# Kernel optimization log

Hardware: AMD Instinct MI355X
Metric: run time of the kernel (lower is better)

## Reference

```python
import jax, jax.numpy as jnp
import numpy as np

N = 4096
FIN = 4096
LOC = 16
H1, H2, HEADS = 120, 50, 4
H1_PER = H1 // HEADS
FILM_Z = 32
SSDB_H = 60
N_HEMI = N // 2
NEG_SLOPE = 0.1
GATE_BIAS = -2.0
MASK_FILL = -9e15


def leaky(x):
    return jax.nn.leaky_relu(x, negative_slope=NEG_SLOPE)


def gat(x, mask, W, a_src, a_dst, bias, concat):
    # x: (N, Fin), W: (H, Fin, O), a_src/a_dst: (H, O), mask: (N, N) bool
    wh = jnp.einsum('nf,hfo->hno', x, W)            # (H, N, O)
    f1 = jnp.einsum('hno,ho->hn', wh, a_src)        # (H, N)
    f2 = jnp.einsum('hno,ho->hn', wh, a_dst)        # (H, N)
    e = leaky(f1[:, :, None] + f2[:, None, :])      # (H, N, N)
    e = jnp.where(mask[None], e, MASK_FILL)
    alpha = jax.nn.softmax(e, axis=-1)
    out = jnp.einsum('hij,hjo->hio', alpha, wh)     # (H, N, O)
    if concat:
        h, n, o = out.shape
        out2 = out.transpose(1, 0, 2).reshape(n, h * o)
    else:
        out2 = out.mean(axis=0)
    return out2 + bias


def _uni(k, shape, stdv):
    return jax.random.uniform(k, shape, jnp.float32, -stdv, stdv)


def setup_inputs() -> dict:
    key = jax.random.key(0)
    ks = jax.random.split(key, 30)
    s1 = 1.0 / np.sqrt(H1_PER)
    s2 = 1.0 / np.sqrt(H2)
    inp = {
        'x_fc': jax.random.normal(ks[0], (N, FIN), jnp.float32),
        'adj': jax.random.randint(ks[1], (N, N), 0, 2, jnp.int32),
        'l_loc': jax.random.uniform(ks[2], (N, LOC), jnp.float32),
        # gat1
        'W1': _uni(ks[3], (HEADS, FIN, H1_PER), s1),
        'a1s': _uni(ks[4], (HEADS, H1_PER), s1),
        'a1d': _uni(ks[5], (HEADS, H1_PER), s1),
        'b1': _uni(ks[6], (H1,), s1),
        # gat2
        'W2': _uni(ks[7], (1, H1, H2), s2),
        'a2s': _uni(ks[8], (1, H2), s2),
        'a2d': _uni(ks[9], (1, H2), s2),
        'b2': _uni(ks[10], (H2,), s2),
        # classifier (no bias)
        'Wc': _uni(ks[11], (2, H2), s2),
        # FiLM trunk
        'Wl1': _uni(ks[12], (FILM_Z, LOC), 1.0 / np.sqrt(LOC)),
        'bl1': _uni(ks[13], (FILM_Z,), 1.0 / np.sqrt(LOC)),
        'Wl2': _uni(ks[14], (FILM_Z, FILM_Z), 1.0 / np.sqrt(FILM_Z)),
        'bl2': _uni(ks[15], (FILM_Z,), 1.0 / np.sqrt(FILM_Z)),
        'Wg': _uni(ks[16], (H2, FILM_Z), 1.0 / np.sqrt(FILM_Z)),
        'bg': _uni(ks[17], (H2,), 1.0 / np.sqrt(FILM_Z)),
        'Wb': _uni(ks[18], (H2, FILM_Z), 1.0 / np.sqrt(FILM_Z)),
        'bb': _uni(ks[19], (H2,), 1.0 / np.sqrt(FILM_Z)),
        'Wgate': _uni(ks[20], (1, FILM_Z), 1.0 / np.sqrt(FILM_Z)),
        'bgate': jnp.full((1,), GATE_BIAS, jnp.float32),
        # SSDB hemi
        'Ws1': _uni(ks[21], (SSDB_H, N_HEMI), 1.0 / np.sqrt(N_HEMI)),
        'bs1': _uni(ks[22], (SSDB_H,), 1.0 / np.sqrt(N_HEMI)),
        'Ws2': _uni(ks[23], (1, SSDB_H), 1.0 / np.sqrt(SSDB_H)),
        'bs2': _uni(ks[24], (1,), 1.0 / np.sqrt(SSDB_H)),
    }
    return inp


def reference(x_fc, adj, l_loc, W1, a1s, a1d, b1, W2, a2s, a2d, b2, Wc,
              Wl1, bl1, Wl2, bl2, Wg, bg, Wb, bb, Wgate, bgate,
              Ws1, bs1, Ws2, bs2):
    mask = adj > 0
    h = leaky(gat(x_fc, mask, W1, a1s, a1d, b1, concat=True))    # (N, 120)
    h = leaky(gat(h, mask, W2, a2s, a2d, b2, concat=False))      # (N, 50)
    # FiLM conditioning
    z = leaky(l_loc @ Wl1.T + bl1)
    z = leaky(z @ Wl2.T + bl2)
    gamma = z @ Wg.T + bg                                        # (N, 50)
    beta = z @ Wb.T + bb                                         # (N, 50)
    g = jax.nn.sigmoid(z @ Wgate.T + bgate)                      # (N, 1)
    cov = jnp.clip(l_loc[:, -1], 0.0, 1.0)                       # coverage_power = 1.0
    g = g * cov[:, None]
    h_fused = h + g * (gamma * h + beta)
    logits = leaky(h_fused @ Wc.T)                               # (N, 2)
    # hemisphere SSDB bias
    t = logits.T                                                 # (2, N)
    ipsi = t[:, :N_HEMI]
    contra = t[:, N_HEMI:2 * N_HEMI]
    h_i = leaky(ipsi @ Ws1.T + bs1)                              # (2, 60)
    h_c = leaky(contra @ Ws1.T + bs1)
    b_i = leaky(h_i @ Ws2.T + bs2)                               # (2, 1)
    b_c = leaky(h_c @ Ws2.T + bs2)
    b_mid = 0.5 * (b_i + b_c)                                    # (2, 1)
    bias_nodes = jnp.concatenate([
        jnp.broadcast_to(b_i.T, (N_HEMI, 2)),
        jnp.broadcast_to(b_c.T, (N_HEMI, 2)),
    ], axis=0)                                                   # n_mid = 0
    logits = logits + bias_nodes
    bias_avg = b_mid[:, 0]                                       # (2,)
    return logits, bias_avg
```

## Files before the change

### kernel.cpp

```cpp
#include <hip/hip_runtime.h>

#define NN 4096
#define HEADS 4
#define H1PER 30
#define H1DIM 120
#define H2DIM 50

typedef short short8_t __attribute__((ext_vector_type(8)));
typedef float f32x4 __attribute__((ext_vector_type(4)));

__device__ __forceinline__ float lrelu(float x) { return x > 0.f ? x : 0.1f * x; }

__device__ __forceinline__ unsigned short bfrne(float x) {
  unsigned u = __float_as_uint(x);
  u += 0x7fffu + ((u >> 16) & 1u);
  return (unsigned short)(u >> 16);
}
__device__ __forceinline__ unsigned bfpk_rne(float lo, float hi) {
  return (unsigned)bfrne(lo) | ((unsigned)bfrne(hi) << 16);
}
__device__ __forceinline__ unsigned bfpk(float lo, float hi) {
  unsigned a = (__float_as_uint(lo) + 0x8000u) >> 16;
  unsigned b = (__float_as_uint(hi) + 0x8000u) & 0xffff0000u;
  return a | b;
}

#define GL16(g, l)                                                                        \
  __builtin_amdgcn_global_load_lds((const __attribute__((address_space(1))) unsigned int*)(g), \
                                   (__attribute__((address_space(3))) unsigned int*)(l), 16, 0, 0)

__global__ __launch_bounds__(256) void k_bits(const int* __restrict__ adj,
                                              unsigned long long* __restrict__ bits) {
  size_t base = (size_t)blockIdx.x * 1024;
  int t = threadIdx.x;
  int v0 = adj[base + t];
  int v1 = adj[base + 256 + t];
  int v2 = adj[base + 512 + t];
  int v3 = adj[base + 768 + t];
  unsigned long long m0 = __ballot(v0 > 0);
  unsigned long long m1 = __ballot(v1 > 0);
  unsigned long long m2 = __ballot(v2 > 0);
  unsigned long long m3 = __ballot(v3 > 0);
  if ((t & 63) == 0) {
    size_t w = (base + t) >> 6;
    bits[w] = m0;
    bits[w + 4] = m1;
    bits[w + 8] = m2;
    bits[w + 12] = m3;
  }
}

__global__ __launch_bounds__(256) void k_prep(const float* __restrict__ W1,
                                              const float* __restrict__ a1s,
                                              const float* __restrict__ a1d,
                                              unsigned short* __restrict__ w1t) {
  int k = blockIdx.x * 256 + threadIdx.x;
#pragma unroll
  for (int h = 0; h < 4; ++h) {
    const float* wp = W1 + ((size_t)h * 4096 + k) * H1PER;
    float fs = 0.f, fd = 0.f;
#pragma unroll
    for (int oo = 0; oo < H1PER; ++oo) {
      float v = wp[oo];
      w1t[(size_t)(h * 30 + oo) * 4096 + k] = bfrne(v);
      fs += v * a1s[h * H1PER + oo];
      fd += v * a1d[h * H1PER + oo];
    }
    w1t[(size_t)(120 + h) * 4096 + k] = bfrne(fs);
    w1t[(size_t)(124 + h) * 4096 + k] = bfrne(fd);
  }
}

__global__ __launch_bounds__(256) void k_gemm1s(const float* __restrict__ x,
                                                const unsigned short* __restrict__ w1t,
                                                float* __restrict__ part) {
  const int t = threadIdx.x;
  const int lane = t & 63, wave = t >> 6;
  const int m = lane & 15, q = lane >> 4;
  const int i0 = blockIdx.x * 32;
  const int kz = blockIdx.y * 512;
  __shared__ float xs[32 * 64];
  const int r0 = (wave & 1) * 16;
  const int ntg0 = (wave >> 1) * 4;
  const int srow0 = wave * 8 + q;
  const int srow1 = srow0 + 4;
  const int sc0 = m ^ (srow0 & 7);
  const int sc1 = m ^ (srow1 & 7);
  const float* gx0 = x + (size_t)(i0 + srow0) * 4096 + kz + sc0 * 4;
  const float* gx1 = x + (size_t)(i0 + srow1) * 4096 + kz + sc1 * 4;
  float* ls0 = &xs[srow0 * 64 + m * 4];
  float* ls1 = &xs[srow1 * 64 + m * 4];
  const int arow = r0 + m;
  const int asw = (m & 7);
  f32x4 acc[4];
#pragma unroll
  for (int nt = 0; nt < 4; ++nt) acc[nt] = (f32x4){0.f, 0.f, 0.f, 0.f};
  for (int it = 0; it < 8; ++it) {
    const int kc = it * 64;
    GL16(gx0 + kc, ls0);
    GL16(gx1 + kc, ls1);
    __syncthreads();
#pragma unroll
    for (int ks2 = 0; ks2 < 2; ++ks2) {
      const int c0 = ks2 * 8 + q * 2;
      float4 a0 = *(const float4*)&xs[arow * 64 + ((c0 ^ asw) * 4)];
      float4 a1 = *(const float4*)&xs[arow * 64 + (((c0 + 1) ^ asw) * 4)];
      union { short8_t v; unsigned u[4]; } A;
      A.u[0] = bfpk_rne(a0.x, a0.y);
      A.u[1] = bfpk_rne(a0.z, a0.w);
      A.u[2] = bfpk_rne(a1.x, a1.y);
      A.u[3] = bfpk_rne(a1.z, a1.w);
      const unsigned short* wp = w1t + (size_t)m * 4096 + kz + kc + ks2 * 32 + q * 8;
#pragma unroll
      for (int nt = 0; nt < 4; ++nt) {
        short8_t B = *(const short8_t*)(wp + (size_t)(ntg0 + nt) * 16 * 4096);
        acc[nt] = __builtin_amdgcn_mfma_f32_16x16x32_bf16(A.v, B, acc[nt], 0, 0, 0);
      }
    }
    __syncthreads();
  }
  float* pp = part + ((size_t)blockIdx.y * 4096 + i0 + r0 + q * 4) * 128 + ntg0 * 16 + m;
#pragma unroll
  for (int nt = 0; nt < 4; ++nt)
#pragma unroll
    for (int r = 0; r < 4; ++r) pp[r * 128 + nt * 16] = acc[nt][r];
}

__global__ __launch_bounds__(256) void k_f1c(const float* __restrict__ part,
                                             unsigned short* __restrict__ whbt,
                                             float* __restrict__ f1, float* __restrict__ f2) {
  const int t = threadIdx.x;
  const int n = blockIdx.x * 16 + (t >> 4);
  const int og = (t & 15) * 8;
  float s[8] = {0.f, 0.f, 0.f, 0.f, 0.f, 0.f, 0.f, 0.f};
  for (int z = 0; z < 8; ++z) {
    const float* pp = part + ((size_t)z * NN + n) * 128 + og;
    float4 u0 = *(const float4*)pp;
    float4 u1 = *(const float4*)(pp + 4);
    s[0] += u0.x; s[1] += u0.y; s[2] += u0.z; s[3] += u0.w;
    s[4] += u1.x; s[5] += u1.y; s[6] += u1.z; s[7] += u1.w;
  }
  if (og < 120) {
#pragma unroll
    for (int j = 0; j < 8; ++j) {
      int o = og + j;
      int h = o / 30, oo = o - h * 30;
      whbt[(size_t)(h * 32 + oo) * NN + n] = bfrne(s[j]);
    }
  } else {
#pragma unroll
    for (int j = 0; j < 4; ++j) {
      f1[(size_t)j * NN + n] = s[j];
      f2[(size_t)j * NN + n] = s[4 + j];
    }
  }
  if ((t & 15) < 8) {
    int h = (t & 15) >> 1, odd = (t & 15) & 1;
    whbt[(size_t)(h * 32 + 30 + odd) * NN + n] = odd ? 0 : 0x3f80;
  }
}

__global__ __launch_bounds__(256) void k_max(const float* __restrict__ v, float* __restrict__ mx) {
  int t = threadIdx.x;
  const float* row = v + (size_t)blockIdx.x * NN;
  float m = -3.0e38f;
  for (int n = t; n < NN; n += 256) m = fmaxf(m, row[n]);
  for (int off = 32; off > 0; off >>= 1) m = fmaxf(m, __shfl_down(m, off));
  __shared__ float ms[4];
  if ((t & 63) == 0) ms[t >> 6] = m;
  __syncthreads();
  if (t == 0) mx[blockIdx.x] = fmaxf(fmaxf(ms[0], ms[1]), fmaxf(ms[2], ms[3]));
}

__global__ __launch_bounds__(256) void k_att1m(const unsigned short* __restrict__ whbt,
                                               const float* __restrict__ f1, const float* __restrict__ f2,
                                               const float* __restrict__ mx,
                                               const unsigned int* __restrict__ bits32,
                                               float* __restrict__ part) {
  const int h = blockIdx.y, js = blockIdx.z;
  const int t = threadIdx.x;
  const int lane = t & 63, wave = t >> 6;
  const int m = lane & 15, q = lane >> 4;
  const int i0 = blockIdx.x * 64 + wave * 16;
  const int jbase = js * 1024;
  const float mxh = mx[h];
  __shared__ float2 es[1024];
  for (int e = t; e < 1024; e += 256) {
    float fv = f2[h * NN + jbase + e] - mxh;
    es[e] = make_float2(__expf(fv), __expf(0.1f * fv));
  }
  __syncthreads();
  const float f1r = f1[h * NN + i0 + m];
  const float s = f1r + mxh;
  const float C1 = __expf(fminf(0.f, 0.9f * s));
  const float C2 = __expf(fminf(0.f, -0.9f * s));
  const float Tr = __expf(-s);
  const unsigned int* brow = bits32 + (size_t)(i0 + m) * 128 + (jbase >> 5);
  const unsigned short* bb0 = whbt + (size_t)(h * 32 + m) * NN + jbase + q * 8;
  const unsigned short* bb1 = bb0 + 16 * NN;
  const float2* fp = es + q * 8;
  f32x4 acc0 = {0.f, 0.f, 0.f, 0.f}, acc1 = {0.f, 0.f, 0.f, 0.f};
  for (int step = 0; step < 32; ++step) {
    const int jl = step * 32;
    unsigned bsel = brow[step] >> (q * 8);
    float4 e01 = *(const float4*)(fp + jl);
    float4 e23 = *(const float4*)(fp + jl + 2);
    float4 e45 = *(const float4*)(fp + jl + 4);
    float4 e67 = *(const float4*)(fp + jl + 6);
    auto sc = [&](float ep, float en, int jj) {
      float wv = (ep > Tr) ? C1 * ep : C2 * en;
      return ((bsel >> jj) & 1u) ? wv : 0.f;
    };
    float w0 = sc(e01.x, e01.y, 0);
    float w1 = sc(e01.z, e01.w, 1);
    float w2 = sc(e23.x, e23.y, 2);
    float w3 = sc(e23.z, e23.w, 3);
    float w4 = sc(e45.x, e45.y, 4);
    float w5 = sc(e45.z, e45.w, 5);
    float w6 = sc(e67.x, e67.y, 6);
    float w7 = sc(e67.z, e67.w, 7);
    union { short8_t v; unsigned u[4]; } A;
    A.u[0] = bfpk(w0, w1);
    A.u[1] = bfpk(w2, w3);
    A.u[2] = bfpk(w4, w5);
    A.u[3] = bfpk(w6, w7);
    short8_t b0 = *(const short8_t*)(bb0 + jl);
    short8_t b1 = *(const short8_t*)(bb1 + jl);
    acc0 = __builtin_amdgcn_mfma_f32_16x16x32_bf16(A.v, b0, acc0, 0, 0, 0);
    acc1 = __builtin_amdgcn_mfma_f32_16x16x32_bf16(A.v, b1, acc1, 0, 0, 0);
  }
  float* pp = part + ((size_t)(js * 4 + h) * NN + i0 + q * 4) * 32 + m;
#pragma unroll
  for (int r = 0; r < 4; ++r) {
    pp[r * 32] = acc0[r];
    pp[r * 32 + 16] = acc1[r];
  }
}

__global__ __launch_bounds__(256) void k_h1(const float* __restrict__ part, const float* __restrict__ b1,
                                            float* __restrict__ h1) {
  int t = threadIdx.x;
  int lane = t & 63;
  int p = lane >> 5, o = lane & 31;
  int id = blockIdx.x * 8 + (t >> 6) * 2 + p;
  int h = id >> 12, n = id & 4095;
  float tot = 0.f;
#pragma unroll
  for (int z = 0; z < 4; ++z) tot += part[((size_t)(z * 4 + h) * NN + n) * 32 + o];
  float l = __shfl(tot, p * 32 + 30);
  if (o < H1PER) h1[(size_t)n * H1DIM + h * H1PER + o] = lrelu(tot / l + b1[h * H1PER + o]);
}

__global__ __launch_bounds__(256) void k_gemm2(const float* __restrict__ h1, const float* __restrict__ W2,
                                               float* __restrict__ wh2) {
  const int n0 = blockIdx.x * 4;
  const int t = threadIdx.x;
  const int o = t & 63, r = t >> 6;
  __shared__ float hs[4][120];
  for (int e = t; e < 4 * H1DIM; e += 256) hs[e / H1DIM][e % H1DIM] = h1[(size_t)n0 * H1DIM + e];
  __syncthreads();
  if (o < H2DIM) {
    float acc = 0.f;
#pragma unroll 4
    for (int k = 0; k < H1DIM; ++k) acc += hs[r][k] * W2[k * H2DIM + o];
    wh2[(size_t)(n0 + r) * H2DIM + o] = acc;
  }
}

__global__ __launch_bounds__(256) void k_f2l2(const float* __restrict__ wh2, const float* __restrict__ a2s,
                                              const float* __restrict__ a2d, float* __restrict__ f1,
                                              float* __restrict__ f2, unsigned short* __restrict__ whbt) {
  int n = blockIdx.x * 256 + threadIdx.x;
  if (n >= NN) return;
  const float* r = wh2 + (size_t)n * H2DIM;
  unsigned short* wb = whbt + n;
  float accs = 0.f, accd = 0.f;
#pragma unroll
  for (int j = 0; j < H2DIM; ++j) {
    float v = r[j];
    wb[j * NN] = bfrne(v);
    accs += v * a2s[j];
    accd += v * a2d[j];
  }
  wb[50 * NN] = 0x3f80;
#pragma unroll
  for (int j = 51; j < 64; ++j) wb[j * NN] = 0;
  f1[n] = accs;
  f2[n] = accd;
}

__global__ __launch_bounds__(256) void k_att2m(const unsigned short* __restrict__ whbt,
                                               const float* __restrict__ f1, const float* __restrict__ f2,
                                               const float* __restrict__ mx,
                                               const unsigned int* __restrict__ bits32,
                                               float* __restrict__ part) {
  const int js = blockIdx.y;
  const int t = threadIdx.x;
  const int lane = t & 63, wave = t >> 6;
  const int m = lane & 15, q = lane >> 4;
  const int i0 = blockIdx.x * 64 + wave * 16;
  const int jbase = js * 512;
  const float mx0 = mx[0];
  __shared__ float2 es[512];
  for (int e = t; e < 512; e += 256) {
    float fv = f2[jbase + e] - mx0;
    es[e] = make_float2(__expf(fv), __expf(0.1f * fv));
  }
  __syncthreads();
  const float f1r = f1[i0 + m];
  const float s = f1r + mx0;
  const float C1 = __expf(fminf(0.f, 0.9f * s));
  const float C2 = __expf(fminf(0.f, -0.9f * s));
  const float Tr = __expf(-s);
  const unsigned int* brow = bits32 + (size_t)(i0 + m) * 128 + (jbase >> 5);
  const unsigned short* bb = whbt + (size_t)m * NN + jbase + q * 8;
  const float2* fp = es + q * 8;
  f32x4 acc[4];
#pragma unroll
  for (int x = 0; x < 4; ++x) acc[x] = (f32x4){0.f, 0.f, 0.f, 0.f};
  for (int step = 0; step < 16; ++step) {
    const int jl = step * 32;
    unsigned bsel = brow[step] >> (q * 8);
    float4 e01 = *(const float4*)(fp + jl);
    float4 e23 = *(const float4*)(fp + jl + 2);
    float4 e45 = *(const float4*)(fp + jl + 4);
    float4 e67 = *(const float4*)(fp + jl + 6);
    auto sc = [&](float ep, float en, int jj) {
      float wv = (ep > Tr) ? C1 * ep : C2 * en;
      return ((bsel >> jj) & 1u) ? wv : 0.f;
    };
    float w0 = sc(e01.x, e01.y, 0);
    float w1 = sc(e01.z, e01.w, 1);
    float w2 = sc(e23.x, e23.y, 2);
    float w3 = sc(e23.z, e23.w, 3);
    float w4 = sc(e45.x, e45.y, 4);
    float w5 = sc(e45.z, e45.w, 5);
    float w6 = sc(e67.x, e67.y, 6);
    float w7 = sc(e67.z, e67.w, 7);
    union { short8_t v; unsigned u[4]; } A;
    A.u[0] = bfpk(w0, w1);
    A.u[1] = bfpk(w2, w3);
    A.u[2] = bfpk(w4, w5);
    A.u[3] = bfpk(w6, w7);
#pragma unroll
    for (int tile = 0; tile < 4; ++tile) {
      short8_t b = *(const short8_t*)(bb + (size_t)tile * 16 * NN + jl);
      acc[tile] = __builtin_amdgcn_mfma_f32_16x16x32_bf16(A.v, b, acc[tile], 0, 0, 0);
    }
  }
  float* pp = part + ((size_t)js * NN + i0 + q * 4) * 64 + m;
#pragma unroll
  for (int tile = 0; tile < 4; ++tile)
#pragma unroll
    for (int r = 0; r < 4; ++r) pp[r * 64 + tile * 16] = acc[tile][r];
}

__global__ __launch_bounds__(256) void k_h2(const float* __restrict__ part, const float* __restrict__ b2,
                                            float* __restrict__ h2) {
  int t = threadIdx.x;
  int n = blockIdx.x * 4 + (t >> 6);
  int o = t & 63;
  const float* p = part + (size_t)n * 64 + o;
  float tot = 0.f;
#pragma unroll
  for (int z = 0; z < 8; ++z) tot += p[(size_t)z * NN * 64];
  float l = __shfl(tot, 50);
  if (o < H2DIM) h2[(size_t)n * H2DIM + o] = lrelu(tot / l + b2[o]);
}

__global__ __launch_bounds__(256) void k_film(const float* __restrict__ l_loc, const float* __restrict__ h2,
                                              const float* __restrict__ Wl1, const float* __restrict__ bl1,
                                              const float* __restrict__ Wl2, const float* __restrict__ bl2,
                                              const float* __restrict__ Wg, const float* __restrict__ bg,
                                              const float* __restrict__ Wb, const float* __restrict__ bb,
                                              const float* __restrict__ Wgate, const float* __restrict__ bgate,
                                              const float* __restrict__ Wc, float* __restrict__ logits) {
  int n = blockIdx.x * 4 + (threadIdx.x >> 6);
  int lane = threadIdx.x & 63;
  int r32 = lane & 31;
  float locv = l_loc[n * 16 + (lane & 15)];
  float cov = __shfl(locv, 15);
  cov = fminf(fmaxf(cov, 0.f), 1.f);
  float a1v = bl1[r32];
#pragma unroll
  for (int j = 0; j < 16; ++j) a1v += Wl1[r32 * 16 + j] * __shfl(locv, j);
  float z1 = lrelu(a1v);
  float a2v = bl2[r32];
#pragma unroll
  for (int j = 0; j < 32; ++j) a2v += Wl2[r32 * 32 + j] * __shfl(z1, j);
  float z2 = lrelu(a2v);
  float gs = bgate[0];
  float gam, bet;
  {
    int o = lane < H2DIM ? lane : 0;
    gam = bg[o];
    bet = bb[o];
#pragma unroll
    for (int j = 0; j < 32; ++j) {
      float zj = __shfl(z2, j);
      gs += Wgate[j] * zj;
      gam += Wg[o * 32 + j] * zj;
      bet += Wb[o * 32 + j] * zj;
    }
  }
  float g = cov / (1.f + __expf(-gs));
  int o = lane < H2DIM ? lane : 0;
  float hv = h2[(size_t)n * H2DIM + o];
  float hf = hv + g * (gam * hv + bet);
  float p0 = lane < H2DIM ? hf * Wc[o] : 0.f;
  float p1 = lane < H2DIM ? hf * Wc[H2DIM + o] : 0.f;
  for (int off = 32; off > 0; off >>= 1) {
    p0 += __shfl_down(p0, off);
    p1 += __shfl_down(p1, off);
  }
  if (lane == 0) {
    logits[n * 2 + 0] = lrelu(p0);
    logits[n * 2 + 1] = lrelu(p1);
  }
}

__global__ __launch_bounds__(64) void k_ssdb1(const float* __restrict__ logits, const float* __restrict__ Ws1,
                                              float* __restrict__ hsum) {
  int combo = blockIdx.y;
  int hemi = combo >> 1, c = combo & 1;
  int k = threadIdx.x;
  if (k >= 60) return;
  int nbase = blockIdx.x * 256;
  const float* wrow = Ws1 + (size_t)k * 2048 + nbase;
  const float* lcol = logits + (size_t)(hemi * 2048 + nbase) * 2 + c;
  float part = 0.f;
  for (int q = 0; q < 256; ++q) part += wrow[q] * lcol[2 * q];
  atomicAdd(&hsum[combo * 60 + k], part);
}

__global__ __launch_bounds__(256) void k_ssdb2(const float* __restrict__ hsum, const float* __restrict__ bs1,
                                               const float* __restrict__ Ws2, const float* __restrict__ bs2,
                                               float* __restrict__ B) {
  int t = threadIdx.x;
  int combo = t >> 6, k = t & 63;
  float part = 0.f;
  if (k < 60) part = lrelu(hsum[combo * 60 + k] + bs1[k]) * Ws2[k];
  for (int off = 32; off > 0; off >>= 1) part += __shfl_down(part, off);
  if (k == 0) B[combo] = lrelu(part + bs2[0]);
}

__global__ __launch_bounds__(256) void k_final(const float* __restrict__ logits, const float* __restrict__ B,
                                               float* __restrict__ out) {
  int id = blockIdx.x * 256 + threadIdx.x;
  if (id < 2 * NN) {
    int n = id >> 1, c = id & 1;
    out[id] = logits[id] + B[(n < 2048 ? 0 : 2) + c];
  } else if (id < 2 * NN + 2) {
    int c = id - 2 * NN;
    out[id] = 0.5f * (B[c] + B[2 + c]);
  }
}

#define OFF_BITS 0
#define OFF_W1T 524288
#define OFF_GP 786432
#define OFF_A1P 786432
#define OFF_A2P 786432
#define OFF_H1 2883584
#define OFF_WH2 3375104
#define OFF_WH2BT 3579904
#define OFF_F12 3710976
#define OFF_F22 3715072
#define OFF_MX2 3719168
#define OFF_H2 3719232
#define OFF_LOG 3924032
#define OFF_HSUM 3932224
#define OFF_B 3932480
#define OFF_WH1BT 9175040
#define OFF_F1A 9437184
#define OFF_F2A 9453568
#define OFF_MX1 9469952

extern "C" void kernel_launch(void* const* d_in, const int* in_sizes, int n_in,
                              void* d_out, int out_size, void* d_ws, size_t ws_size,
                              hipStream_t stream) {
  const float* x_fc  = (const float*)d_in[0];
  const int*   adj   = (const int*)d_in[1];
  const float* l_loc = (const float*)d_in[2];
  const float* W1    = (const float*)d_in[3];
  const float* a1s   = (const float*)d_in[4];
  const float* a1d   = (const float*)d_in[5];
  const float* b1    = (const float*)d_in[6];
  const float* W2    = (const float*)d_in[7];
  const float* a2s   = (const float*)d_in[8];
  const float* a2d   = (const float*)d_in[9];
  const float* b2    = (const float*)d_in[10];
  const float* Wc    = (const float*)d_in[11];
  const float* Wl1   = (const float*)d_in[12];
  const float* bl1   = (const float*)d_in[13];
  const float* Wl2   = (const float*)d_in[14];
  const float* bl2   = (const float*)d_in[15];
  const float* Wg    = (const float*)d_in[16];
  const float* bg    = (const float*)d_in[17];
  const float* Wb    = (const float*)d_in[18];
  const float* bb    = (const float*)d_in[19];
  const float* Wgate = (const float*)d_in[20];
  const float* bgate = (const float*)d_in[21];
  const float* Ws1   = (const float*)d_in[22];
  const float* bs1   = (const float*)d_in[23];
  const float* Ws2   = (const float*)d_in[24];
  const float* bs2   = (const float*)d_in[25];
  float* out = (float*)d_out;
  float* w = (float*)d_ws;
  unsigned long long* bits = (unsigned long long*)(w + OFF_BITS);
  const unsigned int* bits32 = (const unsigned int*)bits;
  unsigned short* wh1bt = (unsigned short*)(w + OFF_WH1BT);
  unsigned short* wh2bt = (unsigned short*)(w + OFF_WH2BT);
  unsigned short* w1t = (unsigned short*)(w + OFF_W1T);

  k_bits<<<NN * NN / 1024, 256, 0, stream>>>(adj, bits);
  k_prep<<<16, 256, 0, stream>>>(W1, a1s, a1d, w1t);
  k_gemm1s<<<dim3(128, 8), 256, 0, stream>>>(x_fc, w1t, w + OFF_GP);
  k_f1c<<<256, 256, 0, stream>>>(w + OFF_GP, wh1bt, w + OFF_F1A, w + OFF_F2A);
  k_max<<<HEADS, 256, 0, stream>>>(w + OFF_F2A, w + OFF_MX1);
  k_att1m<<<dim3(64, HEADS, 4), 256, 0, stream>>>(wh1bt, w + OFF_F1A, w + OFF_F2A,
                                                  w + OFF_MX1, bits32, w + OFF_A1P);
  k_h1<<<2048, 256, 0, stream>>>(w + OFF_A1P, b1, w + OFF_H1);
  k_gemm2<<<NN / 4, 256, 0, stream>>>(w + OFF_H1, W2, w + OFF_WH2);
  k_f2l2<<<NN / 256, 256, 0, stream>>>(w + OFF_WH2, a2s, a2d, w + OFF_F12, w + OFF_F22, wh2bt);
  k_max<<<1, 256, 0, stream>>>(w + OFF_F22, w + OFF_MX2);
  k_att2m<<<dim3(64, 8), 256, 0, stream>>>(wh2bt, w + OFF_F12, w + OFF_F22,
                                           w + OFF_MX2, bits32, w + OFF_A2P);
  k_h2<<<NN / 4, 256, 0, stream>>>(w + OFF_A2P, b2, w + OFF_H2);
  k_film<<<NN / 4, 256, 0, stream>>>(l_loc, w + OFF_H2, Wl1, bl1, Wl2, bl2, Wg, bg, Wb, bb,
                                     Wgate, bgate, Wc, w + OFF_LOG);
  hipMemsetAsync(w + OFF_HSUM, 0, 240 * sizeof(float), stream);
  k_ssdb1<<<dim3(8, 4), 64, 0, stream>>>(w + OFF_LOG, Ws1, w + OFF_HSUM);
  k_ssdb2<<<1, 256, 0, stream>>>(w + OFF_HSUM, bs1, Ws2, bs2, w + OFF_B);
  k_final<<<(2 * NN + 2 + 255) / 256, 256, 0, stream>>>(w + OFF_LOG, w + OFF_B, out);
}
```

Measured before the change: 366.8 us.

## Fuse GAT epilogues, replace max kernels with atomics, pad row strides

```diff
diff --git a/kernel.cpp b/kernel.cpp
--- a/kernel.cpp
+++ b/kernel.cpp
@@ -1,6 +1,8 @@
 #include <hip/hip_runtime.h>
 
 #define NN 4096
+#define NNP 4128
+#define BROW 132
 #define HEADS 4
 #define H1PER 30
 #define H1DIM 120
@@ -24,6 +26,13 @@
   unsigned b = (__float_as_uint(hi) + 0x8000u) & 0xffff0000u;
   return a | b;
 }
+__device__ __forceinline__ unsigned fenc(float x) {
+  unsigned u = __float_as_uint(x);
+  return (u & 0x80000000u) ? ~u : (u | 0x80000000u);
+}
+__device__ __forceinline__ float fdec(unsigned u) {
+  return (u & 0x80000000u) ? __uint_as_float(u ^ 0x80000000u) : __uint_as_float(~u);
+}
 
 #define GL16(g, l)                                                                        \
   __builtin_amdgcn_global_load_lds((const __attribute__((address_space(1))) unsigned int*)(g), \
@@ -31,7 +40,8 @@
 
 __global__ __launch_bounds__(256) void k_bits(const int* __restrict__ adj,
                                               unsigned long long* __restrict__ bits) {
-  size_t base = (size_t)blockIdx.x * 1024;
+  int n = blockIdx.x >> 2, r = blockIdx.x & 3;
+  size_t base = (size_t)n * 4096 + r * 1024;
   int t = threadIdx.x;
   int v0 = adj[base + t];
   int v1 = adj[base + 256 + t];
@@ -42,7 +52,7 @@
   unsigned long long m2 = __ballot(v2 > 0);
   unsigned long long m3 = __ballot(v3 > 0);
   if ((t & 63) == 0) {
-    size_t w = (base + t) >> 6;
+    size_t w = (size_t)n * (BROW / 2) + r * 16 + (t >> 6);
     bits[w] = m0;
     bits[w + 4] = m1;
     bits[w + 8] = m2;
@@ -62,12 +72,12 @@
 #pragma unroll
     for (int oo = 0; oo < H1PER; ++oo) {
       float v = wp[oo];
-      w1t[(size_t)(h * 30 + oo) * 4096 + k] = bfrne(v);
+      w1t[(size_t)(h * 30 + oo) * NNP + k] = bfrne(v);
       fs += v * a1s[h * H1PER + oo];
       fd += v * a1d[h * H1PER + oo];
     }
-    w1t[(size_t)(120 + h) * 4096 + k] = bfrne(fs);
-    w1t[(size_t)(124 + h) * 4096 + k] = bfrne(fd);
+    w1t[(size_t)(120 + h) * NNP + k] = bfrne(fs);
+    w1t[(size_t)(124 + h) * NNP + k] = bfrne(fd);
   }
 }
 
@@ -110,10 +120,10 @@
       A.u[1] = bfpk_rne(a0.z, a0.w);
       A.u[2] = bfpk_rne(a1.x, a1.y);
       A.u[3] = bfpk_rne(a1.z, a1.w);
-      const unsigned short* wp = w1t + (size_t)m * 4096 + kz + kc + ks2 * 32 + q * 8;
+      const unsigned short* wp = w1t + (size_t)m * NNP + kz + kc + ks2 * 32 + q * 8;
 #pragma unroll
       for (int nt = 0; nt < 4; ++nt) {
-        short8_t B = *(const short8_t*)(wp + (size_t)(ntg0 + nt) * 16 * 4096);
+        short8_t B = *(const short8_t*)(wp + (size_t)(ntg0 + nt) * 16 * NNP);
         acc[nt] = __builtin_amdgcn_mfma_f32_16x16x32_bf16(A.v, B, acc[nt], 0, 0, 0);
       }
     }
@@ -128,10 +138,12 @@
 
 __global__ __launch_bounds__(256) void k_f1c(const float* __restrict__ part,
                                              unsigned short* __restrict__ whbt,
-                                             float* __restrict__ f1, float* __restrict__ f2) {
+                                             float* __restrict__ f1, float* __restrict__ f2,
+                                             unsigned* __restrict__ mxu1) {
   const int t = threadIdx.x;
   const int n = blockIdx.x * 16 + (t >> 4);
   const int og = (t & 15) * 8;
+  __shared__ float f2loc[16][4];
   float s[8] = {0.f, 0.f, 0.f, 0.f, 0.f, 0.f, 0.f, 0.f};
   for (int z = 0; z < 8; ++z) {
     const float* pp = part + ((size_t)z * NN + n) * 128 + og;
@@ -145,36 +157,32 @@
     for (int j = 0; j < 8; ++j) {
       int o = og + j;
       int h = o / 30, oo = o - h * 30;
-      whbt[(size_t)(h * 32 + oo) * NN + n] = bfrne(s[j]);
+      whbt[(size_t)(h * 32 + oo) * NNP + n] = bfrne(s[j]);
     }
   } else {
 #pragma unroll
     for (int j = 0; j < 4; ++j) {
       f1[(size_t)j * NN + n] = s[j];
       f2[(size_t)j * NN + n] = s[4 + j];
+      f2loc[t >> 4][j] = s[4 + j];
     }
   }
   if ((t & 15) < 8) {
     int h = (t & 15) >> 1, odd = (t & 15) & 1;
-    whbt[(size_t)(h * 32 + 30 + odd) * NN + n] = odd ? 0 : 0x3f80;
-  }
-}
-
-__global__ __launch_bounds__(256) void k_max(const float* __restrict__ v, float* __restrict__ mx) {
-  int t = threadIdx.x;
-  const float* row = v + (size_t)blockIdx.x * NN;
-  float m = -3.0e38f;
-  for (int n = t; n < NN; n += 256) m = fmaxf(m, row[n]);
-  for (int off = 32; off > 0; off >>= 1) m = fmaxf(m, __shfl_down(m, off));
-  __shared__ float ms[4];
-  if ((t & 63) == 0) ms[t >> 6] = m;
-  __syncthreads();
-  if (t == 0) mx[blockIdx.x] = fmaxf(fmaxf(ms[0], ms[1]), fmaxf(ms[2], ms[3]));
+    whbt[(size_t)(h * 32 + 30 + odd) * NNP + n] = odd ? 0 : 0x3f80;
+  }
+  __syncthreads();
+  if (t < 4) {
+    float m = f2loc[0][t];
+#pragma unroll
+    for (int i = 1; i < 16; ++i) m = fmaxf(m, f2loc[i][t]);
+    atomicMax(&mxu1[t], fenc(m));
+  }
 }
 
 __global__ __launch_bounds__(256) void k_att1m(const unsigned short* __restrict__ whbt,
                                                const float* __restrict__ f1, const float* __restrict__ f2,
-                                               const float* __restrict__ mx,
+                                               const unsigned* __restrict__ mxu1,
                                                const unsigned int* __restrict__ bits32,
                                                float* __restrict__ part) {
   const int h = blockIdx.y, js = blockIdx.z;
@@ -183,7 +191,7 @@
   const int m = lane & 15, q = lane >> 4;
   const int i0 = blockIdx.x * 64 + wave * 16;
   const int jbase = js * 1024;
-  const float mxh = mx[h];
+  const float mxh = fdec(mxu1[h]);
   __shared__ float2 es[1024];
   for (int e = t; e < 1024; e += 256) {
     float fv = f2[h * NN + jbase + e] - mxh;
@@ -195,39 +203,36 @@
   const float C1 = __expf(fminf(0.f, 0.9f * s));
   const float C2 = __expf(fminf(0.f, -0.9f * s));
   const float Tr = __expf(-s);
-  const unsigned int* brow = bits32 + (size_t)(i0 + m) * 128 + (jbase >> 5);
-  const unsigned short* bb0 = whbt + (size_t)(h * 32 + m) * NN + jbase + q * 8;
-  const unsigned short* bb1 = bb0 + 16 * NN;
+  const uint4* brow4 = (const uint4*)(bits32 + (size_t)(i0 + m) * BROW + (jbase >> 5));
+  const unsigned short* bb0 = whbt + (size_t)(h * 32 + m) * NNP + jbase + q * 8;
+  const unsigned short* bb1 = bb0 + 16 * NNP;
   const float2* fp = es + q * 8;
   f32x4 acc0 = {0.f, 0.f, 0.f, 0.f}, acc1 = {0.f, 0.f, 0.f, 0.f};
-  for (int step = 0; step < 32; ++step) {
-    const int jl = step * 32;
-    unsigned bsel = brow[step] >> (q * 8);
-    float4 e01 = *(const float4*)(fp + jl);
-    float4 e23 = *(const float4*)(fp + jl + 2);
-    float4 e45 = *(const float4*)(fp + jl + 4);
-    float4 e67 = *(const float4*)(fp + jl + 6);
-    auto sc = [&](float ep, float en, int jj) {
-      float wv = (ep > Tr) ? C1 * ep : C2 * en;
-      return ((bsel >> jj) & 1u) ? wv : 0.f;
-    };
-    float w0 = sc(e01.x, e01.y, 0);
-    float w1 = sc(e01.z, e01.w, 1);
-    float w2 = sc(e23.x, e23.y, 2);
-    float w3 = sc(e23.z, e23.w, 3);
-    float w4 = sc(e45.x, e45.y, 4);
-    float w5 = sc(e45.z, e45.w, 5);
-    float w6 = sc(e67.x, e67.y, 6);
-    float w7 = sc(e67.z, e67.w, 7);
-    union { short8_t v; unsigned u[4]; } A;
-    A.u[0] = bfpk(w0, w1);
-    A.u[1] = bfpk(w2, w3);
-    A.u[2] = bfpk(w4, w5);
-    A.u[3] = bfpk(w6, w7);
-    short8_t b0 = *(const short8_t*)(bb0 + jl);
-    short8_t b1 = *(const short8_t*)(bb1 + jl);
-    acc0 = __builtin_amdgcn_mfma_f32_16x16x32_bf16(A.v, b0, acc0, 0, 0, 0);
-    acc1 = __builtin_amdgcn_mfma_f32_16x16x32_bf16(A.v, b1, acc1, 0, 0, 0);
+  for (int s4 = 0; s4 < 8; ++s4) {
+    uint4 bq = brow4[s4];
+#pragma unroll
+    for (int sub = 0; sub < 4; ++sub) {
+      const int step = s4 * 4 + sub;
+      const int jl = step * 32;
+      unsigned bsel = (sub == 0 ? bq.x : sub == 1 ? bq.y : sub == 2 ? bq.z : bq.w) >> (q * 8);
+      float4 e01 = *(const float4*)(fp + jl);
+      float4 e23 = *(const float4*)(fp + jl + 2);
+      float4 e45 = *(const float4*)(fp + jl + 4);
+      float4 e67 = *(const float4*)(fp + jl + 6);
+      auto sc = [&](float ep, float en, int jj) {
+        float wv = (ep > Tr) ? C1 * ep : C2 * en;
+        return ((bsel >> jj) & 1u) ? wv : 0.f;
+      };
+      union { short8_t v; unsigned u[4]; } A;
+      A.u[0] = bfpk(sc(e01.x, e01.y, 0), sc(e01.z, e01.w, 1));
+      A.u[1] = bfpk(sc(e23.x, e23.y, 2), sc(e23.z, e23.w, 3));
+      A.u[2] = bfpk(sc(e45.x, e45.y, 4), sc(e45.z, e45.w, 5));
+      A.u[3] = bfpk(sc(e67.x, e67.y, 6), sc(e67.z, e67.w, 7));
+      short8_t b0 = *(const short8_t*)(bb0 + jl);
+      short8_t b1 = *(const short8_t*)(bb1 + jl);
+      acc0 = __builtin_amdgcn_mfma_f32_16x16x32_bf16(A.v, b0, acc0, 0, 0, 0);
+      acc1 = __builtin_amdgcn_mfma_f32_16x16x32_bf16(A.v, b1, acc1, 0, 0, 0);
+    }
   }
   float* pp = part + ((size_t)(js * 4 + h) * NN + i0 + q * 4) * 32 + m;
 #pragma unroll
@@ -237,61 +242,65 @@
   }
 }
 
-__global__ __launch_bounds__(256) void k_h1(const float* __restrict__ part, const float* __restrict__ b1,
-                                            float* __restrict__ h1) {
-  int t = threadIdx.x;
-  int lane = t & 63;
-  int p = lane >> 5, o = lane & 31;
-  int id = blockIdx.x * 8 + (t >> 6) * 2 + p;
-  int h = id >> 12, n = id & 4095;
-  float tot = 0.f;
-#pragma unroll
-  for (int z = 0; z < 4; ++z) tot += part[((size_t)(z * 4 + h) * NN + n) * 32 + o];
-  float l = __shfl(tot, p * 32 + 30);
-  if (o < H1PER) h1[(size_t)n * H1DIM + h * H1PER + o] = lrelu(tot / l + b1[h * H1PER + o]);
-}
-
-__global__ __launch_bounds__(256) void k_gemm2(const float* __restrict__ h1, const float* __restrict__ W2,
-                                               float* __restrict__ wh2) {
-  const int n0 = blockIdx.x * 4;
-  const int t = threadIdx.x;
-  const int o = t & 63, r = t >> 6;
-  __shared__ float hs[4][120];
-  for (int e = t; e < 4 * H1DIM; e += 256) hs[e / H1DIM][e % H1DIM] = h1[(size_t)n0 * H1DIM + e];
-  __syncthreads();
+__global__ __launch_bounds__(256) void k_fuseA(const float* __restrict__ part, const float* __restrict__ b1,
+                                               const float* __restrict__ W2, const float* __restrict__ a2s,
+                                               const float* __restrict__ a2d,
+                                               unsigned short* __restrict__ whbt2,
+                                               float* __restrict__ f1b, float* __restrict__ f2b,
+                                               unsigned* __restrict__ mxu2) {
+  const int t = threadIdx.x;
+  __shared__ float W2s[H1DIM * H2DIM];
+  __shared__ float h1s[4][124];
+  __shared__ float f2red[4];
+  for (int e = t; e < H1DIM * H2DIM; e += 256) W2s[e] = W2[e];
+  const int wv = t >> 6, lane = t & 63;
+  const int n = blockIdx.x * 4 + wv;
+  const int h = lane >> 4, o2 = (lane & 15) * 2;
+  float tot0 = 0.f, tot1 = 0.f;
+#pragma unroll
+  for (int z = 0; z < 4; ++z) {
+    const float* pp = part + ((size_t)(z * 4 + h) * NN + n) * 32 + o2;
+    float2 u = *(const float2*)pp;
+    tot0 += u.x;
+    tot1 += u.y;
+  }
+  float l = __shfl(tot0, h * 16 + 15);
+  float inv = 1.f / l;
+  if (o2 < 30) {
+    h1s[wv][h * 30 + o2] = lrelu(tot0 * inv + b1[h * 30 + o2]);
+    h1s[wv][h * 30 + o2 + 1] = lrelu(tot1 * inv + b1[h * 30 + o2 + 1]);
+  }
+  __syncthreads();
+  const int o = lane;
+  float acc = 0.f;
   if (o < H2DIM) {
-    float acc = 0.f;
+    const float* hr = h1s[wv];
 #pragma unroll 4
-    for (int k = 0; k < H1DIM; ++k) acc += hs[r][k] * W2[k * H2DIM + o];
-    wh2[(size_t)(n0 + r) * H2DIM + o] = acc;
-  }
-}
-
-__global__ __launch_bounds__(256) void k_f2l2(const float* __restrict__ wh2, const float* __restrict__ a2s,
-                                              const float* __restrict__ a2d, float* __restrict__ f1,
-                                              float* __restrict__ f2, unsigned short* __restrict__ whbt) {
-  int n = blockIdx.x * 256 + threadIdx.x;
-  if (n >= NN) return;
-  const float* r = wh2 + (size_t)n * H2DIM;
-  unsigned short* wb = whbt + n;
-  float accs = 0.f, accd = 0.f;
-#pragma unroll
-  for (int j = 0; j < H2DIM; ++j) {
-    float v = r[j];
-    wb[j * NN] = bfrne(v);
-    accs += v * a2s[j];
-    accd += v * a2d[j];
-  }
-  wb[50 * NN] = 0x3f80;
-#pragma unroll
-  for (int j = 51; j < 64; ++j) wb[j * NN] = 0;
-  f1[n] = accs;
-  f2[n] = accd;
-}
-
-__global__ __launch_bounds__(256) void k_att2m(const unsigned short* __restrict__ whbt,
-                                               const float* __restrict__ f1, const float* __restrict__ f2,
-                                               const float* __restrict__ mx,
+    for (int k = 0; k < H1DIM; ++k) acc += hr[k] * W2s[k * H2DIM + o];
+  }
+  unsigned short wbv = (o < H2DIM) ? bfrne(acc) : (o == H2DIM ? (unsigned short)0x3f80 : (unsigned short)0);
+  whbt2[(size_t)o * NNP + n] = wbv;
+  float ps = (o < H2DIM) ? acc * a2s[o] : 0.f;
+  float pd = (o < H2DIM) ? acc * a2d[o] : 0.f;
+  for (int off = 32; off > 0; off >>= 1) {
+    ps += __shfl_down(ps, off);
+    pd += __shfl_down(pd, off);
+  }
+  if (lane == 0) {
+    f1b[n] = ps;
+    f2b[n] = pd;
+    f2red[wv] = pd;
+  }
+  __syncthreads();
+  if (t == 0) {
+    float m = fmaxf(fmaxf(f2red[0], f2red[1]), fmaxf(f2red[2], f2red[3]));
+    atomicMax(mxu2, fenc(m));
+  }
+}
+
+__global__ __launch_bounds__(256) void k_att2m(const unsigned short* __restrict__ whbt2,
+                                               const float* __restrict__ f1b, const float* __restrict__ f2b,
+                                               const unsigned* __restrict__ mxu2,
                                                const unsigned int* __restrict__ bits32,
                                                float* __restrict__ part) {
   const int js = blockIdx.y;
@@ -300,52 +309,49 @@
   const int m = lane & 15, q = lane >> 4;
   const int i0 = blockIdx.x * 64 + wave * 16;
   const int jbase = js * 512;
-  const float mx0 = mx[0];
+  const float mx0 = fdec(mxu2[0]);
   __shared__ float2 es[512];
   for (int e = t; e < 512; e += 256) {
-    float fv = f2[jbase + e] - mx0;
+    float fv = f2b[jbase + e] - mx0;
     es[e] = make_float2(__expf(fv), __expf(0.1f * fv));
   }
   __syncthreads();
-  const float f1r = f1[i0 + m];
+  const float f1r = f1b[i0 + m];
   const float s = f1r + mx0;
   const float C1 = __expf(fminf(0.f, 0.9f * s));
   const float C2 = __expf(fminf(0.f, -0.9f * s));
   const float Tr = __expf(-s);
-  const unsigned int* brow = bits32 + (size_t)(i0 + m) * 128 + (jbase >> 5);
-  const unsigned short* bb = whbt + (size_t)m * NN + jbase + q * 8;
+  const uint4* brow4 = (const uint4*)(bits32 + (size_t)(i0 + m) * BROW + (jbase >> 5));
+  const unsigned short* bb = whbt2 + (size_t)m * NNP + jbase + q * 8;
   const float2* fp = es + q * 8;
   f32x4 acc[4];
 #pragma unroll
   for (int x = 0; x < 4; ++x) acc[x] = (f32x4){0.f, 0.f, 0.f, 0.f};
-  for (int step = 0; step < 16; ++step) {
-    const int jl = step * 32;
-    unsigned bsel = brow[step] >> (q * 8);
-    float4 e01 = *(const float4*)(fp + jl);
-    float4 e23 = *(const float4*)(fp + jl + 2);
-    float4 e45 = *(const float4*)(fp + jl + 4);
-    float4 e67 = *(const float4*)(fp + jl + 6);
-    auto sc = [&](float ep, float en, int jj) {
-      float wv = (ep > Tr) ? C1 * ep : C2 * en;
-      return ((bsel >> jj) & 1u) ? wv : 0.f;
-    };
-    float w0 = sc(e01.x, e01.y, 0);
-    float w1 = sc(e01.z, e01.w, 1);
-    float w2 = sc(e23.x, e23.y, 2);
-    float w3 = sc(e23.z, e23.w, 3);
-    float w4 = sc(e45.x, e45.y, 4);
-    float w5 = sc(e45.z, e45.w, 5);
-    float w6 = sc(e67.x, e67.y, 6);
-    float w7 = sc(e67.z, e67.w, 7);
-    union { short8_t v; unsigned u[4]; } A;
-    A.u[0] = bfpk(w0, w1);
-    A.u[1] = bfpk(w2, w3);
-    A.u[2] = bfpk(w4, w5);
-    A.u[3] = bfpk(w6, w7);
-#pragma unroll
-    for (int tile = 0; tile < 4; ++tile) {
-      short8_t b = *(const short8_t*)(bb + (size_t)tile * 16 * NN + jl);
-      acc[tile] = __builtin_amdgcn_mfma_f32_16x16x32_bf16(A.v, b, acc[tile], 0, 0, 0);
+  for (int s4 = 0; s4 < 4; ++s4) {
+    uint4 bq = brow4[s4];
+#pragma unroll
+    for (int sub = 0; sub < 4; ++sub) {
+      const int step = s4 * 4 + sub;
+      const int jl = step * 32;
+      unsigned bsel = (sub == 0 ? bq.x : sub == 1 ? bq.y : sub == 2 ? bq.z : bq.w) >> (q * 8);
+      float4 e01 = *(const float4*)(fp + jl);
+      float4 e23 = *(const float4*)(fp + jl + 2);
+      float4 e45 = *(const float4*)(fp + jl + 4);
+      float4 e67 = *(const float4*)(fp + jl + 6);
+      auto sc = [&](float ep, float en, int jj) {
+        float wv = (ep > Tr) ? C1 * ep : C2 * en;
+        return ((bsel >> jj) & 1u) ? wv : 0.f;
+      };
+      union { short8_t v; unsigned u[4]; } A;
+      A.u[0] = bfpk(sc(e01.x, e01.y, 0), sc(e01.z, e01.w, 1));
+      A.u[1] = bfpk(sc(e23.x, e23.y, 2), sc(e23.z, e23.w, 3));
+      A.u[2] = bfpk(sc(e45.x, e45.y, 4), sc(e45.z, e45.w, 5));
+      A.u[3] = bfpk(sc(e67.x, e67.y, 6), sc(e67.z, e67.w, 7));
+#pragma unroll
+      for (int tile = 0; tile < 4; ++tile) {
+        short8_t b = *(const short8_t*)(bb + (size_t)tile * 16 * NNP + jl);
+        acc[tile] = __builtin_amdgcn_mfma_f32_16x16x32_bf16(A.v, b, acc[tile], 0, 0, 0);
+      }
     }
   }
   float* pp = part + ((size_t)js * NN + i0 + q * 4) * 64 + m;
@@ -355,28 +361,23 @@
     for (int r = 0; r < 4; ++r) pp[r * 64 + tile * 16] = acc[tile][r];
 }
 
-__global__ __launch_bounds__(256) void k_h2(const float* __restrict__ part, const float* __restrict__ b2,
-                                            float* __restrict__ h2) {
-  int t = threadIdx.x;
-  int n = blockIdx.x * 4 + (t >> 6);
-  int o = t & 63;
-  const float* p = part + (size_t)n * 64 + o;
+__global__ __launch_bounds__(256) void k_fuseB(const float* __restrict__ part, const float* __restrict__ b2,
+                                               const float* __restrict__ l_loc,
+                                               const float* __restrict__ Wl1, const float* __restrict__ bl1,
+                                               const float* __restrict__ Wl2, const float* __restrict__ bl2,
+                                               const float* __restrict__ Wg, const float* __restrict__ bg,
+                                               const float* __restrict__ Wb, const float* __restrict__ bb,
+                                               const float* __restrict__ Wgate, const float* __restrict__ bgate,
+                                               const float* __restrict__ Wc, float* __restrict__ logits) {
+  const int t = threadIdx.x;
+  const int wv = t >> 6, lane = t & 63;
+  const int n = blockIdx.x * 4 + wv;
+  const float* p = part + (size_t)n * 64 + lane;
   float tot = 0.f;
 #pragma unroll
   for (int z = 0; z < 8; ++z) tot += p[(size_t)z * NN * 64];
   float l = __shfl(tot, 50);
-  if (o < H2DIM) h2[(size_t)n * H2DIM + o] = lrelu(tot / l + b2[o]);
-}
-
-__global__ __launch_bounds__(256) void k_film(const float* __restrict__ l_loc, const float* __restrict__ h2,
-                                              const float* __restrict__ Wl1, const float* __restrict__ bl1,
-                                              const float* __restrict__ Wl2, const float* __restrict__ bl2,
-                                              const float* __restrict__ Wg, const float* __restrict__ bg,
-                                              const float* __restrict__ Wb, const float* __restrict__ bb,
-                                              const float* __restrict__ Wgate, const float* __restrict__ bgate,
-                                              const float* __restrict__ Wc, float* __restrict__ logits) {
-  int n = blockIdx.x * 4 + (threadIdx.x >> 6);
-  int lane = threadIdx.x & 63;
+  float hv = (lane < H2DIM) ? lrelu(tot / l + b2[lane]) : 0.f;
   int r32 = lane & 31;
   float locv = l_loc[n * 16 + (lane & 15)];
   float cov = __shfl(locv, 15);
@@ -404,9 +405,8 @@
     }
   }
   float g = cov / (1.f + __expf(-gs));
+  float hf = hv + g * (gam * hv + bet);
   int o = lane < H2DIM ? lane : 0;
-  float hv = h2[(size_t)n * H2DIM + o];
-  float hf = hv + g * (gam * hv + bet);
   float p0 = lane < H2DIM ? hf * Wc[o] : 0.f;
   float p1 = lane < H2DIM ? hf * Wc[H2DIM + o] : 0.f;
   for (int off = 32; off > 0; off >>= 1) {
@@ -419,62 +419,57 @@
   }
 }
 
-__global__ __launch_bounds__(64) void k_ssdb1(const float* __restrict__ logits, const float* __restrict__ Ws1,
-                                              float* __restrict__ hsum) {
-  int combo = blockIdx.y;
-  int hemi = combo >> 1, c = combo & 1;
-  int k = threadIdx.x;
-  if (k >= 60) return;
-  int nbase = blockIdx.x * 256;
-  const float* wrow = Ws1 + (size_t)k * 2048 + nbase;
-  const float* lcol = logits + (size_t)(hemi * 2048 + nbase) * 2 + c;
-  float part = 0.f;
-  for (int q = 0; q < 256; ++q) part += wrow[q] * lcol[2 * q];
-  atomicAdd(&hsum[combo * 60 + k], part);
-}
-
-__global__ __launch_bounds__(256) void k_ssdb2(const float* __restrict__ hsum, const float* __restrict__ bs1,
+__global__ __launch_bounds__(1024) void k_ssdb(const float* __restrict__ logits,
+                                               const float* __restrict__ Ws1, const float* __restrict__ bs1,
                                                const float* __restrict__ Ws2, const float* __restrict__ bs2,
-                                               float* __restrict__ B) {
-  int t = threadIdx.x;
-  int combo = t >> 6, k = t & 63;
-  float part = 0.f;
-  if (k < 60) part = lrelu(hsum[combo * 60 + k] + bs1[k]) * Ws2[k];
-  for (int off = 32; off > 0; off >>= 1) part += __shfl_down(part, off);
-  if (k == 0) B[combo] = lrelu(part + bs2[0]);
-}
-
-__global__ __launch_bounds__(256) void k_final(const float* __restrict__ logits, const float* __restrict__ B,
                                                float* __restrict__ out) {
-  int id = blockIdx.x * 256 + threadIdx.x;
-  if (id < 2 * NN) {
-    int n = id >> 1, c = id & 1;
-    out[id] = logits[id] + B[(n < 2048 ? 0 : 2) + c];
-  } else if (id < 2 * NN + 2) {
-    int c = id - 2 * NN;
-    out[id] = 0.5f * (B[c] + B[2 + c]);
-  }
+  const int t = threadIdx.x;
+  __shared__ float lg[8192];
+  __shared__ float hs[256];
+  __shared__ float Bs[4];
+  for (int e = t; e < 8192; e += 1024) lg[e] = logits[e];
+  __syncthreads();
+  if (t < 960) {
+    int item = t >> 2, seg = t & 3;
+    int k = item % 60, combo = item / 60;
+    int hemi = combo >> 1, c = combo & 1;
+    const float* wr = Ws1 + (size_t)k * 2048 + seg * 512;
+    const float* lc = logits + (size_t)(hemi * 2048 + seg * 512) * 2 + c;
+    float pacc = 0.f;
+    for (int q2 = 0; q2 < 512; ++q2) pacc += wr[q2] * lc[2 * q2];
+    pacc += __shfl_down(pacc, 1);
+    pacc += __shfl_down(pacc, 2);
+    if (seg == 0) hs[item] = pacc;
+  }
+  __syncthreads();
+  if (t < 256) {
+    int combo = t >> 6, k2 = t & 63;
+    float v = (k2 < 60) ? lrelu(hs[combo * 60 + k2] + bs1[k2]) * Ws2[k2] : 0.f;
+    for (int off = 32; off > 0; off >>= 1) v += __shfl_down(v, off);
+    if (k2 == 0) Bs[combo] = lrelu(v + bs2[0]);
+  }
+  __syncthreads();
+  for (int e = t; e < 8192; e += 1024) {
+    int nn = e >> 1, c = e & 1;
+    out[e] = lg[e] + Bs[(nn < 2048 ? 0 : 2) + c];
+  }
+  if (t == 0) out[8192] = 0.5f * (Bs[0] + Bs[2]);
+  if (t == 1) out[8193] = 0.5f * (Bs[1] + Bs[3]);
 }
 
 #define OFF_BITS 0
-#define OFF_W1T 524288
-#define OFF_GP 786432
-#define OFF_A1P 786432
-#define OFF_A2P 786432
-#define OFF_H1 2883584
-#define OFF_WH2 3375104
-#define OFF_WH2BT 3579904
-#define OFF_F12 3710976
-#define OFF_F22 3715072
-#define OFF_MX2 3719168
-#define OFF_H2 3719232
-#define OFF_LOG 3924032
-#define OFF_HSUM 3932224
-#define OFF_B 3932480
-#define OFF_WH1BT 9175040
-#define OFF_F1A 9437184
-#define OFF_F2A 9453568
-#define OFF_MX1 9469952
+#define OFF_W1T 540672
+#define OFF_GP 804864
+#define OFF_A1P 804864
+#define OFF_A2P 804864
+#define OFF_WH1BT 4999168
+#define OFF_F1A 5263360
+#define OFF_F2A 5279744
+#define OFF_WH2BT 5296128
+#define OFF_F12 5428224
+#define OFF_F22 5432320
+#define OFF_LOG 5436416
+#define OFF_MX 5444608
 
 extern "C" void kernel_launch(void* const* d_in, const int* in_sizes, int n_in,
                               void* d_out, int out_size, void* d_ws, size_t ws_size,
@@ -512,25 +507,20 @@
   unsigned short* wh1bt = (unsigned short*)(w + OFF_WH1BT);
   unsigned short* wh2bt = (unsigned short*)(w + OFF_WH2BT);
   unsigned short* w1t = (unsigned short*)(w + OFF_W1T);
-
+  unsigned* mxu = (unsigned*)(w + OFF_MX);
+
+  hipMemsetAsync(mxu, 0, 8 * sizeof(unsigned), stream);
   k_bits<<<NN * NN / 1024, 256, 0, stream>>>(adj, bits);
   k_prep<<<16, 256, 0, stream>>>(W1, a1s, a1d, w1t);
   k_gemm1s<<<dim3(128, 8), 256, 0, stream>>>(x_fc, w1t, w + OFF_GP);
-  k_f1c<<<256, 256, 0, stream>>>(w + OFF_GP, wh1bt, w + OFF_F1A, w + OFF_F2A);
-  k_max<<<HEADS, 256, 0, stream>>>(w + OFF_F2A, w + OFF_MX1);
+  k_f1c<<<256, 256, 0, stream>>>(w + OFF_GP, wh1bt, w + OFF_F1A, w + OFF_F2A, mxu);
   k_att1m<<<dim3(64, HEADS, 4), 256, 0, stream>>>(wh1bt, w + OFF_F1A, w + OFF_F2A,
-                                                  w + OFF_MX1, bits32, w + OFF_A1P);
-  k_h1<<<2048, 256, 0, stream>>>(w + OFF_A1P, b1, w + OFF_H1);
-  k_gemm2<<<NN / 4, 256, 0, stream>>>(w + OFF_H1, W2, w + OFF_WH2);
-  k_f2l2<<<NN / 256, 256, 0, stream>>>(w + OFF_WH2, a2s, a2d, w + OFF_F12, w + OFF_F22, wh2bt);
-  k_max<<<1, 256, 0, stream>>>(w + OFF_F22, w + OFF_MX2);
+                                                  mxu, bits32, w + OFF_A1P);
+  k_fuseA<<<1024, 256, 0, stream>>>(w + OFF_A1P, b1, W2, a2s, a2d, wh2bt,
+                                    w + OFF_F12, w + OFF_F22, mxu + 4);
   k_att2m<<<dim3(64, 8), 256, 0, stream>>>(wh2bt, w + OFF_F12, w + OFF_F22,
-                                           w + OFF_MX2, bits32, w + OFF_A2P);
-  k_h2<<<NN / 4, 256, 0, stream>>>(w + OFF_A2P, b2, w + OFF_H2);
-  k_film<<<NN / 4, 256, 0, stream>>>(l_loc, w + OFF_H2, Wl1, bl1, Wl2, bl2, Wg, bg, Wb, bb,
-                                     Wgate, bgate, Wc, w + OFF_LOG);
-  hipMemsetAsync(w + OFF_HSUM, 0, 240 * sizeof(float), stream);
-  k_ssdb1<<<dim3(8, 4), 64, 0, stream>>>(w + OFF_LOG, Ws1, w + OFF_HSUM);
-  k_ssdb2<<<1, 256, 0, stream>>>(w + OFF_HSUM, bs1, Ws2, bs2, w + OFF_B);
-  k_final<<<(2 * NN + 2 + 255) / 256, 256, 0, stream>>>(w + OFF_LOG, w + OFF_B, out);
-}
+                                           mxu + 4, bits32, w + OFF_A2P);
+  k_fuseB<<<1024, 256, 0, stream>>>(w + OFF_A2P, b2, l_loc, Wl1, bl1, Wl2, bl2,
+                                    Wg, bg, Wb, bb, Wgate, bgate, Wc, w + OFF_LOG);
+  k_ssdb<<<1, 1024, 0, stream>>>(w + OFF_LOG, Ws1, bs1, Ws2, bs2, out);
+}
```

Measured after the change: 424.6 us. +15.7%, slower.
